# Optimization experiments

Measured on AMD Instinct MI355X. Metric: run time of the kernel, lower is better.

Reference implementation:

```python
import jax, jax.numpy as jnp
import numpy as np

B, L, D, N, NBLK = 16, 2048, 256, 64, 6  # 6 S4D layers: blocks 1,2,3,5 + 2 inner layers of FS4Ddeq


def setup_inputs() -> dict:
    key = jax.random.key(0)
    ks = jax.random.split(key, 12)
    x = jax.random.normal(ks[0], (B, L), dtype=jnp.float32)
    W_emb = jax.random.normal(ks[1], (1, D), dtype=jnp.float32) * 0.1
    b_emb = jnp.zeros((D,), jnp.float32)
    # S4D parameters, stacked over the 6 layers
    log_dt = jax.random.uniform(ks[2], (NBLK, D), minval=float(np.log(1e-3)), maxval=float(np.log(1e-1)), dtype=jnp.float32)
    logAre = jnp.full((NBLK, D, N), float(np.log(0.5)), jnp.float32)
    Aim = jnp.broadcast_to(jnp.pi * jnp.arange(N, dtype=jnp.float32), (NBLK, D, N)) * jnp.ones((NBLK, D, N), jnp.float32)
    Cre = jax.random.normal(ks[3], (NBLK, D, N), dtype=jnp.float32) * (0.5 ** 0.5)
    Cim = jax.random.normal(ks[4], (NBLK, D, N), dtype=jnp.float32) * (0.5 ** 0.5)
    Dskip = jax.random.normal(ks[5], (NBLK, D), dtype=jnp.float32)
    Wout = jax.random.normal(ks[6], (NBLK, D, D), dtype=jnp.float32) / np.sqrt(D)
    bout = jnp.zeros((NBLK, D), jnp.float32)
    gamma = jnp.ones((NBLK, D), jnp.float32)
    beta = jnp.zeros((NBLK, D), jnp.float32)
    # feedforward of the FS4Ddeq block (feed_size=[B,L,emb_dim], feed_act='relu')
    feed_W1 = jax.random.normal(ks[7], (D, D), dtype=jnp.float32) / np.sqrt(D)
    feed_b1 = jnp.zeros((D,), jnp.float32)
    feed_W2 = jax.random.normal(ks[8], (D, D), dtype=jnp.float32) / np.sqrt(D)
    feed_b2 = jnp.zeros((D,), jnp.float32)
    fc_W = jax.random.normal(ks[9], (D, 2), dtype=jnp.float32) / np.sqrt(D)
    fc_b = jnp.zeros((2,), jnp.float32)
    return dict(x=x, W_emb=W_emb, b_emb=b_emb, log_dt=log_dt, logAre=logAre, Aim=Aim,
                Cre=Cre, Cim=Cim, Dskip=Dskip, Wout=Wout, bout=bout, gamma=gamma, beta=beta,
                feed_W1=feed_W1, feed_b1=feed_b1, feed_W2=feed_W2, feed_b2=feed_b2,
                fc_W=fc_W, fc_b=fc_b)


def _s4d_block(h, log_dt, logAre, Aim, Cre, Cim, Dskip, Wout, bout, gamma, beta):
    """Pre-norm (BN eval-mode) -> diagonal SSM (ZOH, FFT conv) -> GELU -> Linear -> residual."""
    _, Lh, _ = h.shape
    z = gamma * h + beta  # BatchNorm in eval mode with identity running stats
    dt = jnp.exp(log_dt)[:, None]                      # [D,1]
    A = -jnp.exp(logAre) + 1j * Aim                    # [D,N] diagonal state matrix
    dtA = dt * A                                       # [D,N]
    C = (Cre + 1j * Cim) * (jnp.exp(dtA) - 1.0) / A    # ZOH-discretized C*B
    # Vandermonde kernel K[d,l] = 2*Re sum_n C[d,n] * exp(dtA[d,n])^l
    vand = jnp.exp(dtA[:, :, None] * jnp.arange(Lh, dtype=jnp.float32))  # [D,N,L]
    K = 2.0 * jnp.einsum('dn,dnl->dl', C, vand).real   # [D,L]
    u = jnp.transpose(z, (0, 2, 1))                    # [B,D,L]
    kf = jnp.fft.rfft(K, n=2 * Lh)
    uf = jnp.fft.rfft(u, n=2 * Lh)
    y = jnp.fft.irfft(uf * kf, n=2 * Lh)[..., :Lh]     # causal conv
    y = y + Dskip[:, None] * u                         # feedthrough D
    y = jax.nn.gelu(jnp.transpose(y, (0, 2, 1)))       # [B,L,D]
    y = jnp.einsum('bld,de->ble', y, Wout) + bout      # output projection
    return y + h                                       # skip connection


def reference(x, W_emb, b_emb, log_dt, logAre, Aim, Cre, Cim, Dskip, Wout, bout,
              gamma, beta, feed_W1, feed_b1, feed_W2, feed_b2, fc_W, fc_b):
    h = x[..., None] @ W_emb + b_emb  # nn.Linear(1, emb_dim): [B,L,D]
    # layers 1,2,3,5: S4D blocks (dropout is identity in eval mode)
    for i in range(4):
        h = _s4d_block(h, log_dt[i], logAre[i], Aim[i], Cre[i], Cim[i],
                       Dskip[i], Wout[i], bout[i], gamma[i], beta[i])
    # layer4: FS4Ddeq_model with layers=2 inner S4D blocks + relu feed net + final relu + skip
    r = h
    for i in (4, 5):
        h = _s4d_block(h, log_dt[i], logAre[i], Aim[i], Cre[i], Cim[i],
                       Dskip[i], Wout[i], bout[i], gamma[i], beta[i])
    h = jax.nn.relu(h @ feed_W1 + feed_b1) @ feed_W2 + feed_b2
    h = jax.nn.relu(h + r)
    mean_y = jnp.mean(h, axis=1)       # [B,D]
    logits = mean_y @ fc_W + fc_b      # [B,2]
    return logits
```

## Files before the change

kernel.cpp:

```cpp
#include <hip/hip_runtime.h>
#include <hip/hip_fp16.h>
#include <math.h>

#define B_ 16
#define L_ 2048
#define D_ 256
#define N_ 64
#define NBLK_ 6
#define LC_ 128
#define NC_ 16

typedef _Float16 half8 __attribute__((ext_vector_type(8)));
typedef float f32x4 __attribute__((ext_vector_type(4)));

__device__ __forceinline__ unsigned short f2h(float f) {
  _Float16 h = (_Float16)f;
  return *(unsigned short*)&h;
}
__device__ __forceinline__ float h2f(unsigned short u) {
  _Float16 h = *(_Float16*)&u;
  return (float)h;
}

__global__ void precompute_kernel(const float* __restrict__ log_dt,
                                  const float* __restrict__ logAre,
                                  const float* __restrict__ Aim,
                                  const float* __restrict__ Cre,
                                  const float* __restrict__ Cim,
                                  float* __restrict__ wbuf,
                                  float* __restrict__ c2buf,
                                  float* __restrict__ wlbuf) {
  int idx = blockIdx.x * blockDim.x + threadIdx.x;
  if (idx >= NBLK_ * D_ * N_) return;
  int blk = idx >> 14;
  int rem = idx & 16383;
  int d = rem >> 6;
  int n = rem & 63;
  float dt   = expf(log_dt[blk * D_ + d]);
  float are  = -expf(logAre[idx]);
  float aim  = Aim[idx];
  float dtar = dt * are, dtai = dt * aim;
  float er = expf(dtar);
  float wr = er * cosf(dtai);
  float wi = er * sinf(dtai);
  float inv = 1.0f / (are * are + aim * aim);
  float wm1r = wr - 1.0f;
  float br = (wm1r * are + wi * aim) * inv;
  float bi = (wi * are - wm1r * aim) * inv;
  float crv = Cre[idx], civ = Cim[idx];
  float c2r = 2.0f * (crv * br - civ * bi);
  float c2i = 2.0f * (crv * bi + civ * br);
  float eL = expf((float)LC_ * dtar);
  float angL = (float)LC_ * dtai;
  float* wb = wbuf + (size_t)((blk << 8) + d) * 128;
  wb[n] = wr; wb[64 + n] = wi;
  float* cb = c2buf + (size_t)((blk << 8) + d) * 128;
  cb[n] = c2r; cb[64 + n] = c2i;
  wlbuf[2 * idx] = eL * cosf(angL); wlbuf[2 * idx + 1] = eL * sinf(angL);
}

__global__ void embed_kernel(const float* __restrict__ x, const float* __restrict__ wemb,
                             const float* __restrict__ bemb, unsigned short* __restrict__ H) {
  int tid = blockIdx.x * blockDim.x + threadIdx.x;
  if (tid >= B_ * L_ * D_) return;
  int d = tid & (D_ - 1);
  int lg = tid >> 8;
  H[tid] = f2h(fmaf(x[lg], wemb[d], bemb[d]));
}

__global__ __launch_bounds__(256) void trans_h_ut(const unsigned short* __restrict__ H,
                                                  unsigned short* __restrict__ UT) {
  __shared__ __align__(16) unsigned short lds[64][136];
  int bi = blockIdx.x;
  int bc = bi >> 2, dq = bi & 3;
  int b = bc >> 4, ch = bc & 15;
  int tid = threadIdx.x;
  const unsigned short* src = H + ((size_t)(b * L_ + ch * 128)) * D_ + dq * 64;
  int tau0 = tid >> 4;
  int dl = (tid & 15) << 2;
  for (int tt = 0; tt < 128; tt += 16) {
    ushort4 v = *(const ushort4*)(src + (size_t)(tt + tau0) * D_ + dl);
    lds[dl + 0][tt + tau0] = v.x;
    lds[dl + 1][tt + tau0] = v.y;
    lds[dl + 2][tt + tau0] = v.z;
    lds[dl + 3][tt + tau0] = v.w;
  }
  __syncthreads();
  int r = tid >> 2, seg = (tid & 3) << 5;
  unsigned short* dst = UT + ((size_t)((dq * 64 + r) * 256 + bc)) * 128 + seg;
  const unsigned short* srow = &lds[r][seg];
  *(uint4*)(dst + 0)  = *(const uint4*)(srow + 0);
  *(uint4*)(dst + 8)  = *(const uint4*)(srow + 8);
  *(uint4*)(dst + 16) = *(const uint4*)(srow + 16);
  *(uint4*)(dst + 24) = *(const uint4*)(srow + 24);
}

__global__ __launch_bounds__(256) void scan_fused(
    const unsigned short* __restrict__ UT,
    const float* __restrict__ WB, const float* __restrict__ C2B,
    const float* __restrict__ WLB,
    const float* __restrict__ gamma_, const float* __restrict__ beta_,
    const float* __restrict__ dskip,
    unsigned short* __restrict__ GT, int blk) {
  __shared__ __align__(16) unsigned short SLl[256 * 136];
  __shared__ __align__(16) unsigned short Bm1[128 * 136];
  __shared__ __align__(16) unsigned short Bm2[128 * 136];
  __shared__ __align__(16) unsigned short AsB[128 * 40];
  __shared__ float wc[256];
  __shared__ float Kt[128];
  __shared__ float Pb[128];
  __shared__ float Sb[128];
  _Float16* As = (_Float16*)AsB;
  int d = blockIdx.x;
  int tid = threadIdx.x, lane = tid & 63, w = tid >> 6;
  int wm = (w & 1) << 6, wn = (w >> 1) << 6;
  int r = tid & 127, sg = (tid >> 7) << 4;
  int cn = lane & 15, rq = lane >> 4;
  int ko = (lane >> 4) << 3;
  const unsigned short* Au = UT + (size_t)d * 256 * 128;

  if (tid < 128) wc[tid] = WB[(size_t)((blk << 8) + d) * 128 + tid];
  else           wc[tid] = C2B[(size_t)((blk << 8) + d) * 128 + (tid - 128)];
  __syncthreads();
  int n = tid & 63, tj = tid >> 6;
  float gd = gamma_[blk * D_ + d], bd = beta_[blk * D_ + d], dsk = dskip[blk * D_ + d];
  {
    float wr = wc[n], wi = wc[64 + n];
    float c2r = wc[128 + n], c2i = wc[192 + n];
    int j0 = tj << 5;
    float pr = 1.f, pi = 0.f, br = wr, bi = wi;
    int e = j0;
    while (e) {
      if (e & 1) { float tt = pr * br - pi * bi; pi = pr * bi + pi * br; pr = tt; }
      float t2 = br * br - bi * bi; bi = 2.f * br * bi; br = t2;
      e >>= 1;
    }
    for (int k2 = 0; k2 < 32; ++k2) {
      int j = j0 + k2;
      Bm1[n * 136 + (127 - j)]        = f2h(gd * pr);
      Bm1[(64 + n) * 136 + (127 - j)] = f2h(-gd * pi);
      float qr = pr * wr - pi * wi, qi = pr * wi + pi * wr;
      Bm2[j * 136 + n]      = f2h(c2r * qr - c2i * qi);
      Bm2[j * 136 + 64 + n] = f2h(c2r * qi + c2i * qr);
      float kc = c2r * pr - c2i * pi;
#pragma unroll
      for (int off = 1; off < 64; off <<= 1) kc += __shfl_xor(kc, off);
      if (n == 0) Kt[j] = kc + (j == 0 ? dsk : 0.f);
      pr = qr; pi = qi;
    }
  }
  if (tid < 64) {
    const float* wlp = WLB + (((size_t)((blk << 8) + d)) * 64 + tid) * 2;
    float wlr = wlp[0], wli = wlp[1];
    float nr = wlr - 1.f, ni = wli;
    float dr2 = wc[tid] - 1.f, di = wc[64 + tid];
    float iv = 1.f / (dr2 * dr2 + di * di);
    Sb[tid]      = bd * ((nr * dr2 + ni * di) * iv);
    Sb[64 + tid] = bd * (-((ni * dr2 - nr * di) * iv));
  }
  __syncthreads();
  if (tid < 128) {
    float ps = 0.f;
    for (int t2 = 0; t2 <= tid; ++t2) ps += Kt[t2];
    Pb[tid] = bd * ps;
  }

  for (int mh = 0; mh < 2; ++mh) {
    const unsigned short* Ab = Au + (size_t)(mh << 7) * 128;
    f32x4 acc[4][4];
#pragma unroll
    for (int a = 0; a < 4; ++a)
#pragma unroll
      for (int b2 = 0; b2 < 4; ++b2) acc[a][b2] = (f32x4){0.f, 0.f, 0.f, 0.f};
    uint4 a0 = *(const uint4*)(Ab + (size_t)r * 128 + sg);
    uint4 a1 = *(const uint4*)(Ab + (size_t)r * 128 + sg + 8);
    for (int kc = 0; kc < 128; kc += 32) {
      __syncthreads();
      *(uint4*)&As[r * 40 + sg] = a0; *(uint4*)&As[r * 40 + sg + 8] = a1;
      __syncthreads();
      if (kc < 96) {
        a0 = *(const uint4*)(Ab + (size_t)r * 128 + kc + 32 + sg);
        a1 = *(const uint4*)(Ab + (size_t)r * 128 + kc + 32 + sg + 8);
      }
      half8 af[4], bf4[4];
#pragma unroll
      for (int mf = 0; mf < 4; ++mf) af[mf] = *(const half8*)&As[(wm + (mf << 4) + cn) * 40 + ko];
#pragma unroll
      for (int nf = 0; nf < 4; ++nf)
        bf4[nf] = *(const half8*)((const _Float16*)Bm1 + (wn + (nf << 4) + cn) * 136 + kc + ko);
#pragma unroll
      for (int mf = 0; mf < 4; ++mf)
#pragma unroll
        for (int nf = 0; nf < 4; ++nf)
          acc[mf][nf] = __builtin_amdgcn_mfma_f32_16x16x32_f16(af[mf], bf4[nf], acc[mf][nf], 0, 0, 0);
    }
#pragma unroll
    for (int nf = 0; nf < 4; ++nf) {
      int nl = wn + (nf << 4) + cn;
      float sb = Sb[nl];
#pragma unroll
      for (int mf = 0; mf < 4; ++mf)
#pragma unroll
        for (int rr = 0; rr < 4; ++rr) {
          int row = (mh << 7) + wm + (mf << 4) + (rq << 2) + rr;
          SLl[row * 136 + nl] = f2h(acc[mf][nf][rr] + sb);
        }
    }
  }
  __syncthreads();

  for (int task = tid; task < 1024; task += 256) {
    int b = task >> 6, nn = task & 63;
    const float* wlp = WLB + (((size_t)((blk << 8) + d)) * 64 + nn) * 2;
    float wlr = wlp[0], wli = wlp[1];
    float Sr = 0.f, Sj = 0.f;
    for (int c = 0; c < NC_; ++c) {
      int row = (b << 4) + c;
      float tr2 = h2f(SLl[row * 136 + nn]);
      float tj2 = h2f(SLl[row * 136 + 64 + nn]);
      SLl[row * 136 + nn]      = f2h(Sr);
      SLl[row * 136 + 64 + nn] = f2h(Sj);
      float nSr = fmaf(wlr, Sr, fmaf(wli, Sj, tr2));
      Sj = fmaf(-wli, Sr, fmaf(wlr, Sj, tj2));
      Sr = nSr;
    }
  }
  __syncthreads();

  {
    int chunk = tid & 15, rg = tid >> 4;
#pragma unroll
    for (int it = 0; it < 8; ++it) {
      int trow = (it << 4) + rg;
      int tau0 = chunk << 3;
      unsigned short v[8];
#pragma unroll
      for (int i = 0; i < 8; ++i) {
        int tau = tau0 + i;
        v[i] = (tau <= trow) ? f2h(gd * Kt[trow - tau]) : (unsigned short)0;
      }
      *(uint4*)(Bm1 + (size_t)trow * 136 + tau0) = *(uint4*)v;
    }
  }
  __syncthreads();

  for (int mh = 0; mh < 2; ++mh) {
    const unsigned short* Ab = Au + (size_t)(mh << 7) * 128;
    const _Float16* SA = (const _Float16*)SLl + (size_t)(mh << 7) * 136;
    f32x4 acc[4][4];
#pragma unroll
    for (int a = 0; a < 4; ++a)
#pragma unroll
      for (int b2 = 0; b2 < 4; ++b2) acc[a][b2] = (f32x4){0.f, 0.f, 0.f, 0.f};
    uint4 a0 = *(const uint4*)(Ab + (size_t)r * 128 + sg);
    uint4 a1 = *(const uint4*)(Ab + (size_t)r * 128 + sg + 8);
    for (int kb = 0; kb < 8; ++kb) {
      int kc = (kb & 3) << 5;
      half8 af[4], bf4[4];
      if (kb < 4) {
        __syncthreads();
        *(uint4*)&As[r * 40 + sg] = a0; *(uint4*)&As[r * 40 + sg + 8] = a1;
        __syncthreads();
        if (kb < 3) {
          int kc2 = (kb + 1) << 5;
          a0 = *(const uint4*)(Ab + (size_t)r * 128 + kc2 + sg);
          a1 = *(const uint4*)(Ab + (size_t)r * 128 + kc2 + sg + 8);
        }
#pragma unroll
        for (int mf = 0; mf < 4; ++mf) af[mf] = *(const half8*)&As[(wm + (mf << 4) + cn) * 40 + ko];
#pragma unroll
        for (int nf = 0; nf < 4; ++nf)
          bf4[nf] = *(const half8*)((const _Float16*)Bm1 + (wn + (nf << 4) + cn) * 136 + kc + ko);
      } else {
#pragma unroll
        for (int mf = 0; mf < 4; ++mf)
          af[mf] = *(const half8*)&SA[(wm + (mf << 4) + cn) * 136 + kc + ko];
#pragma unroll
        for (int nf = 0; nf < 4; ++nf)
          bf4[nf] = *(const half8*)((const _Float16*)Bm2 + (wn + (nf << 4) + cn) * 136 + kc + ko);
      }
#pragma unroll
      for (int mf = 0; mf < 4; ++mf)
#pragma unroll
        for (int nf = 0; nf < 4; ++nf)
          acc[mf][nf] = __builtin_amdgcn_mfma_f32_16x16x32_f16(af[mf], bf4[nf], acc[mf][nf], 0, 0, 0);
    }
    __syncthreads();
    unsigned short* epi = SLl + (size_t)(mh << 7) * 136;
#pragma unroll
    for (int nf = 0; nf < 4; ++nf) {
      int nl = wn + (nf << 4) + cn;
      float pb2 = Pb[nl];
#pragma unroll
      for (int mf = 0; mf < 4; ++mf)
#pragma unroll
        for (int rr = 0; rr < 4; ++rr) {
          int ml = wm + (mf << 4) + (rq << 2) + rr;
          float xx = acc[mf][nf][rr] + pb2;
          float x3 = xx * xx * xx;
          float inner = 0.7978845608028654f * fmaf(0.044715f, x3, xx);
          float e = __expf(-2.f * fabsf(inner));
          float th = (1.f - e) / (1.f + e);
          th = copysignf(th, inner);
          epi[ml * 136 + nl] = f2h(0.5f * xx * (1.f + th));
        }
    }
    __syncthreads();
    int mr = tid >> 1, hf = (tid & 1) << 6;
    size_t gb = ((size_t)d * 256 + (mh << 7) + mr) * 128 + hf;
#pragma unroll
    for (int k = 0; k < 8; ++k)
      *(uint4*)(GT + gb + k * 8) = *(const uint4*)&epi[mr * 136 + hf + k * 8];
  }
}

__global__ void wprep_kernel(const float* __restrict__ Wout, const float* __restrict__ fW1,
                             const float* __restrict__ fW2, unsigned short* __restrict__ WT) {
  __shared__ float tile[64][65];
  int wv = blockIdx.x >> 4;
  int tk = (blockIdx.x >> 2) & 3;
  int tn = blockIdx.x & 3;
  const float* src = (wv < 6) ? (Wout + (size_t)wv * 65536) : (wv == 6 ? fW1 : fW2);
  int r = threadIdx.x >> 4;
  int c = (threadIdx.x & 15) << 2;
  for (int rr = 0; rr < 64; rr += 16) {
    float4 v = *(const float4*)(src + (size_t)(tk * 64 + r + rr) * 256 + tn * 64 + c);
    tile[r + rr][c] = v.x; tile[r + rr][c + 1] = v.y;
    tile[r + rr][c + 2] = v.z; tile[r + rr][c + 3] = v.w;
  }
  __syncthreads();
  for (int rr = 0; rr < 64; rr += 16) {
    int n = r + rr;
    ushort4 o;
    o.x = f2h(tile[c + 0][n]); o.y = f2h(tile[c + 1][n]);
    o.z = f2h(tile[c + 2][n]); o.w = f2h(tile[c + 3][n]);
    *(ushort4*)(WT + (size_t)wv * 65536 + (size_t)(tn * 64 + n) * 256 + tk * 64 + c) = o;
  }
}

__global__ __launch_bounds__(256, 2) void gemm_gt(const unsigned short* __restrict__ GT,
    const unsigned short* __restrict__ Wt, const float* __restrict__ bias,
    const unsigned short* __restrict__ res, unsigned short* __restrict__ hout,
    unsigned short* __restrict__ ut_next) {
  __shared__ __align__(16) unsigned short smem[18432];
  unsigned short* As = smem;
  unsigned short* Bs = smem + 9216;
  int tid = threadIdx.x;
  int bid = blockIdx.x;
  int bc = bid & 255;
  int m0 = bc * 128, n0 = (bid >> 8) << 7;
  int lane = tid & 63, w = tid >> 6;
  int wm = (w & 1) << 6, wn = (w >> 1) << 6;
  int rb = tid >> 3, cb = (tid & 7) << 3;
  int dr = tid >> 2, sg = (tid & 3) << 5;
  f32x4 acc[4][4];
#pragma unroll
  for (int mf = 0; mf < 4; ++mf)
#pragma unroll
    for (int nf = 0; nf < 4; ++nf) acc[mf][nf] = (f32x4){0.f, 0.f, 0.f, 0.f};

  uint4 gv[4], bv[4];
  {
    const uint4* grow = (const uint4*)(GT + ((size_t)(dr * 256 + bc)) * 128 + sg);
    gv[0] = grow[0]; gv[1] = grow[1]; gv[2] = grow[2]; gv[3] = grow[3];
#pragma unroll
    for (int rr = 0; rr < 4; ++rr)
      bv[rr] = *(const uint4*)(Wt + (size_t)(n0 + rb + rr * 32) * 256 + cb);
  }
  for (int kb = 0; kb < 4; ++kb) {
    __syncthreads();
    const unsigned short* pv = (const unsigned short*)gv;
#pragma unroll
    for (int i = 0; i < 32; ++i) As[(sg + i) * 72 + dr] = pv[i];
#pragma unroll
    for (int rr = 0; rr < 4; ++rr) *(uint4*)&Bs[(rb + rr * 32) * 72 + cb] = bv[rr];
    __syncthreads();
    if (kb < 3) {
      int k0 = (kb + 1) << 6;
      const uint4* grow = (const uint4*)(GT + ((size_t)((k0 + dr) * 256 + bc)) * 128 + sg);
      gv[0] = grow[0]; gv[1] = grow[1]; gv[2] = grow[2]; gv[3] = grow[3];
#pragma unroll
      for (int rr = 0; rr < 4; ++rr)
        bv[rr] = *(const uint4*)(Wt + (size_t)(n0 + rb + rr * 32) * 256 + k0 + cb);
    }
#pragma unroll
    for (int kw = 0; kw < 2; ++kw) {
      int ko = (kw << 5) + ((lane >> 4) << 3);
      half8 af[4], bfr[4];
#pragma unroll
      for (int mf = 0; mf < 4; ++mf)
        af[mf] = *(const half8*)&As[(wm + (mf << 4) + (lane & 15)) * 72 + ko];
#pragma unroll
      for (int nf = 0; nf < 4; ++nf)
        bfr[nf] = *(const half8*)&Bs[(wn + (nf << 4) + (lane & 15)) * 72 + ko];
#pragma unroll
      for (int mf = 0; mf < 4; ++mf)
#pragma unroll
        for (int nf = 0; nf < 4; ++nf)
          acc[mf][nf] = __builtin_amdgcn_mfma_f32_16x16x32_f16(af[mf], bfr[nf], acc[mf][nf], 0, 0, 0);
    }
  }
  int cn = lane & 15, rq = lane >> 4;
  __syncthreads();
  unsigned short* epi = smem;
#pragma unroll
  for (int nf = 0; nf < 4; ++nf) {
    int nl = wn + (nf << 4) + cn;
    float bv2 = bias[n0 + nl];
#pragma unroll
    for (int mf = 0; mf < 4; ++mf)
#pragma unroll
      for (int r = 0; r < 4; ++r) {
        int ml = wm + (mf << 4) + (rq << 2) + r;
        float v = acc[mf][nf][r] + bv2 + h2f(res[(size_t)(m0 + ml) * 256 + n0 + nl]);
        epi[ml * 136 + nl] = f2h(v);
      }
  }
  __syncthreads();
  {
    int mr = tid >> 1, hf = (tid & 1) << 6;
    unsigned short* dst = hout + (size_t)(m0 + mr) * 256 + n0 + hf;
    const unsigned short* srow = epi + mr * 136 + hf;
#pragma unroll
    for (int k = 0; k < 8; ++k) *(uint4*)(dst + k * 8) = *(const uint4*)(srow + k * 8);
  }
  if (ut_next) {
    int nl = tid >> 1, h2 = (tid & 1) << 6;
    unsigned short* dst = ut_next + ((size_t)(n0 + nl) * 256 + bc) * 128 + h2;
#pragma unroll
    for (int k = 0; k < 8; ++k) {
      unsigned short v8[8];
#pragma unroll
      for (int e = 0; e < 8; ++e) v8[e] = epi[(h2 + k * 8 + e) * 136 + nl];
      *(uint4*)(dst + k * 8) = *(uint4*)v8;
    }
  }
}

__global__ __launch_bounds__(256, 2) void gemm_ffn(const unsigned short* __restrict__ A,
    const unsigned short* __restrict__ Wt, const float* __restrict__ bias,
    const unsigned short* __restrict__ res, unsigned short* __restrict__ outp) {
  __shared__ __align__(16) unsigned short smem[18432];
  unsigned short* As = smem;
  unsigned short* Bs = smem + 9216;
  int tid = threadIdx.x;
  int bid = blockIdx.x;
  int m0 = (bid & 255) << 7, n0 = (bid >> 8) << 7;
  int lane = tid & 63, w = tid >> 6;
  int wm = (w & 1) << 6, wn = (w >> 1) << 6;
  int r0 = tid >> 3;
  int c0 = (tid & 7) << 3;
  f32x4 acc[4][4];
#pragma unroll
  for (int mf = 0; mf < 4; ++mf)
#pragma unroll
    for (int nf = 0; nf < 4; ++nf) acc[mf][nf] = (f32x4){0.f, 0.f, 0.f, 0.f};

  uint4 av[4], bv[4];
#pragma unroll
  for (int rr = 0; rr < 4; ++rr) {
    int r = r0 + rr * 32;
    av[rr] = *(const uint4*)(A + (size_t)(m0 + r) * 256 + c0);
    bv[rr] = *(const uint4*)(Wt + (size_t)(n0 + r) * 256 + c0);
  }
  for (int kb = 0; kb < 4; ++kb) {
    __syncthreads();
#pragma unroll
    for (int rr = 0; rr < 4; ++rr) {
      int r = r0 + rr * 32;
      *(uint4*)&As[r * 72 + c0] = av[rr];
      *(uint4*)&Bs[r * 72 + c0] = bv[rr];
    }
    __syncthreads();
    if (kb < 3) {
      int k0 = (kb + 1) << 6;
#pragma unroll
      for (int rr = 0; rr < 4; ++rr) {
        int r = r0 + rr * 32;
        av[rr] = *(const uint4*)(A + (size_t)(m0 + r) * 256 + k0 + c0);
        bv[rr] = *(const uint4*)(Wt + (size_t)(n0 + r) * 256 + k0 + c0);
      }
    }
#pragma unroll
    for (int kw = 0; kw < 2; ++kw) {
      int ko = (kw << 5) + ((lane >> 4) << 3);
      half8 af[4], bfr[4];
#pragma unroll
      for (int mf = 0; mf < 4; ++mf)
        af[mf] = *(const half8*)&As[(wm + (mf << 4) + (lane & 15)) * 72 + ko];
#pragma unroll
      for (int nf = 0; nf < 4; ++nf)
        bfr[nf] = *(const half8*)&Bs[(wn + (nf << 4) + (lane & 15)) * 72 + ko];
#pragma unroll
      for (int mf = 0; mf < 4; ++mf)
#pragma unroll
        for (int nf = 0; nf < 4; ++nf)
          acc[mf][nf] = __builtin_amdgcn_mfma_f32_16x16x32_f16(af[mf], bfr[nf], acc[mf][nf], 0, 0, 0);
    }
  }
  int cn = lane & 15, rq = lane >> 4;
  __syncthreads();
  unsigned short* epi = smem;
#pragma unroll
  for (int nf = 0; nf < 4; ++nf) {
    int nl = wn + (nf << 4) + cn;
#pragma unroll
    for (int r = 0; r < 4; ++r) {
#pragma unroll
      for (int mf = 0; mf < 4; ++mf) {
        int ml = wm + (mf << 4) + (rq << 2) + r;
        epi[ml * 136 + nl] = f2h(acc[mf][nf][r]);
      }
    }
  }
  __syncthreads();
  int mr = tid >> 1, hf = (tid & 1) << 6;
  unsigned short* dst = outp + (size_t)(m0 + mr) * 256 + n0 + hf;
#pragma unroll
  for (int k = 0; k < 8; ++k) {
    uint4 c = *(const uint4*)&epi[mr * 136 + hf + k * 8];
    uint4 rv = (uint4){0, 0, 0, 0};
    if (res) rv = *(const uint4*)(res + (size_t)(m0 + mr) * 256 + n0 + hf + k * 8);
    const unsigned short* cp = (const unsigned short*)&c;
    const unsigned short* rp = (const unsigned short*)&rv;
    unsigned short o8[8];
#pragma unroll
    for (int e = 0; e < 8; ++e) {
      float v = h2f(cp[e]) + bias[n0 + hf + k * 8 + e];
      if (res) v += h2f(rp[e]);
      o8[e] = f2h(fmaxf(v, 0.f));
    }
    *(uint4*)(dst + k * 8) = *(uint4*)o8;
  }
}

__global__ void head1_kernel(const unsigned short* __restrict__ H, float* __restrict__ part) {
  int b = blockIdx.x, ls = blockIdx.y, d = threadIdx.x;
  const unsigned short* p = H + ((size_t)(b * L_ + ls * 128)) * D_ + d;
  float sum = 0.f;
  for (int l = 0; l < 128; ++l) sum += h2f(p[(size_t)l * D_]);
  part[(b * 16 + ls) * D_ + d] = sum;
}

__global__ void head2_kernel(const float* __restrict__ part, const float* __restrict__ fcW,
                             const float* __restrict__ fcb, float* __restrict__ out) {
  int b = blockIdx.x, d = threadIdx.x;
  float sum = 0.f;
  for (int i = 0; i < 16; ++i) sum += part[(b * 16 + i) * D_ + d];
  __shared__ float meanv[D_];
  meanv[d] = sum * (1.0f / (float)L_);
  __syncthreads();
  if (d < 2) {
    float accv = fcb[d];
    for (int k = 0; k < D_; ++k) accv = fmaf(meanv[k], fcW[k * 2 + d], accv);
    out[b * 2 + d] = accv;
  }
}

extern "C" void kernel_launch(void* const* d_in, const int* in_sizes, int n_in,
                              void* d_out, int out_size, void* d_ws, size_t ws_size,
                              hipStream_t stream) {
  const float* x      = (const float*)d_in[0];
  const float* W_emb  = (const float*)d_in[1];
  const float* b_emb  = (const float*)d_in[2];
  const float* log_dt = (const float*)d_in[3];
  const float* logAre = (const float*)d_in[4];
  const float* Aim    = (const float*)d_in[5];
  const float* Cre    = (const float*)d_in[6];
  const float* Cim    = (const float*)d_in[7];
  const float* Dskip  = (const float*)d_in[8];
  const float* Wout   = (const float*)d_in[9];
  const float* bout   = (const float*)d_in[10];
  const float* gamma_ = (const float*)d_in[11];
  const float* beta_  = (const float*)d_in[12];
  const float* fW1    = (const float*)d_in[13];
  const float* fb1    = (const float*)d_in[14];
  const float* fW2    = (const float*)d_in[15];
  const float* fb2    = (const float*)d_in[16];
  const float* fcW    = (const float*)d_in[17];
  const float* fcb    = (const float*)d_in[18];
  float* outp = (float*)d_out;

  const size_t HSZ = (size_t)B_ * L_ * D_;
  float* WB     = (float*)d_ws;
  float* C2B    = WB + (size_t)NBLK_ * D_ * 128;
  float* WLB    = C2B + (size_t)NBLK_ * D_ * 128;
  unsigned short* H   = (unsigned short*)(WLB + (size_t)NBLK_ * D_ * N_ * 2);
  unsigned short* R   = H + HSZ;
  unsigned short* UT  = R + HSZ;
  unsigned short* GT  = UT + HSZ;
  unsigned short* Gbf = GT;
  unsigned short* WT  = GT + HSZ;

  precompute_kernel<<<(NBLK_ * D_ * N_ + 255) / 256, 256, 0, stream>>>(
      log_dt, logAre, Aim, Cre, Cim, WB, C2B, WLB);
  wprep_kernel<<<128, 256, 0, stream>>>(Wout, fW1, fW2, WT);
  embed_kernel<<<(B_ * L_ * D_ + 255) / 256, 256, 0, stream>>>(x, W_emb, b_emb, H);
  trans_h_ut<<<1024, 256, 0, stream>>>(H, UT);

  const unsigned short* hin_t[6]  = {H, H, H, H, R, H};
  unsigned short*       hout_t[6] = {H, H, H, R, H, H};
  for (int i = 0; i < 6; ++i) {
    scan_fused<<<256, 256, 0, stream>>>(UT, WB, C2B, WLB, gamma_, beta_, Dskip, GT, i);
    gemm_gt<<<512, 256, 0, stream>>>(
        GT, WT + (size_t)i * 65536, bout + i * D_, hin_t[i], hout_t[i],
        (i < 5) ? UT : nullptr);
  }
  gemm_ffn<<<512, 256, 0, stream>>>(H, WT + (size_t)6 * 65536, fb1, nullptr, Gbf);
  gemm_ffn<<<512, 256, 0, stream>>>(Gbf, WT + (size_t)7 * 65536, fb2, R, H);
  head1_kernel<<<dim3(16, 16), 256, 0, stream>>>(H, WB);
  head2_kernel<<<16, 256, 0, stream>>>(WB, fcW, fcb, outp);
}
```

Before: 610.5 us.

## Widen scan_fused to 512 threads covering both row halves at once

```diff
diff --git a/kernel.cpp b/kernel.cpp
--- a/kernel.cpp
+++ b/kernel.cpp
@@ -95,7 +95,7 @@
   *(uint4*)(dst + 24) = *(const uint4*)(srow + 24);
 }
 
-__global__ __launch_bounds__(256) void scan_fused(
+__global__ __launch_bounds__(512) void scan_fused(
     const unsigned short* __restrict__ UT,
     const float* __restrict__ WB, const float* __restrict__ C2B,
     const float* __restrict__ WLB,
@@ -105,7 +105,7 @@
   __shared__ __align__(16) unsigned short SLl[256 * 136];
   __shared__ __align__(16) unsigned short Bm1[128 * 136];
   __shared__ __align__(16) unsigned short Bm2[128 * 136];
-  __shared__ __align__(16) unsigned short AsB[128 * 40];
+  __shared__ __align__(16) unsigned short AsB[256 * 40];
   __shared__ float wc[256];
   __shared__ float Kt[128];
   __shared__ float Pb[128];
@@ -113,21 +113,22 @@
   _Float16* As = (_Float16*)AsB;
   int d = blockIdx.x;
   int tid = threadIdx.x, lane = tid & 63, w = tid >> 6;
-  int wm = (w & 1) << 6, wn = (w >> 1) << 6;
-  int r = tid & 127, sg = (tid >> 7) << 4;
+  int wm = (w & 3) << 6;
+  int wn = (w >> 2) << 6;
+  int r = tid & 255, sg = (tid >> 8) << 4;
   int cn = lane & 15, rq = lane >> 4;
-  int ko = (lane >> 4) << 3;
+  int ko = rq << 3;
   const unsigned short* Au = UT + (size_t)d * 256 * 128;
 
   if (tid < 128) wc[tid] = WB[(size_t)((blk << 8) + d) * 128 + tid];
-  else           wc[tid] = C2B[(size_t)((blk << 8) + d) * 128 + (tid - 128)];
-  __syncthreads();
-  int n = tid & 63, tj = tid >> 6;
+  else if (tid < 256) wc[tid] = C2B[(size_t)((blk << 8) + d) * 128 + (tid - 128)];
+  __syncthreads();
+  int n = tid & 63;
   float gd = gamma_[blk * D_ + d], bd = beta_[blk * D_ + d], dsk = dskip[blk * D_ + d];
   {
     float wr = wc[n], wi = wc[64 + n];
     float c2r = wc[128 + n], c2i = wc[192 + n];
-    int j0 = tj << 5;
+    int j0 = (tid >> 6) << 4;
     float pr = 1.f, pi = 0.f, br = wr, bi = wi;
     int e = j0;
     while (e) {
@@ -135,7 +136,7 @@
       float t2 = br * br - bi * bi; bi = 2.f * br * bi; br = t2;
       e >>= 1;
     }
-    for (int k2 = 0; k2 < 32; ++k2) {
+    for (int k2 = 0; k2 < 16; ++k2) {
       int j = j0 + k2;
       Bm1[n * 136 + (127 - j)]        = f2h(gd * pr);
       Bm1[(64 + n) * 136 + (127 - j)] = f2h(-gd * pi);
@@ -165,22 +166,21 @@
     Pb[tid] = bd * ps;
   }
 
-  for (int mh = 0; mh < 2; ++mh) {
-    const unsigned short* Ab = Au + (size_t)(mh << 7) * 128;
+  {
     f32x4 acc[4][4];
 #pragma unroll
     for (int a = 0; a < 4; ++a)
 #pragma unroll
       for (int b2 = 0; b2 < 4; ++b2) acc[a][b2] = (f32x4){0.f, 0.f, 0.f, 0.f};
-    uint4 a0 = *(const uint4*)(Ab + (size_t)r * 128 + sg);
-    uint4 a1 = *(const uint4*)(Ab + (size_t)r * 128 + sg + 8);
+    uint4 a0 = *(const uint4*)(Au + (size_t)r * 128 + sg);
+    uint4 a1 = *(const uint4*)(Au + (size_t)r * 128 + sg + 8);
     for (int kc = 0; kc < 128; kc += 32) {
       __syncthreads();
       *(uint4*)&As[r * 40 + sg] = a0; *(uint4*)&As[r * 40 + sg + 8] = a1;
       __syncthreads();
       if (kc < 96) {
-        a0 = *(const uint4*)(Ab + (size_t)r * 128 + kc + 32 + sg);
-        a1 = *(const uint4*)(Ab + (size_t)r * 128 + kc + 32 + sg + 8);
+        a0 = *(const uint4*)(Au + (size_t)r * 128 + kc + 32 + sg);
+        a1 = *(const uint4*)(Au + (size_t)r * 128 + kc + 32 + sg + 8);
       }
       half8 af[4], bf4[4];
 #pragma unroll
@@ -202,14 +202,14 @@
       for (int mf = 0; mf < 4; ++mf)
 #pragma unroll
         for (int rr = 0; rr < 4; ++rr) {
-          int row = (mh << 7) + wm + (mf << 4) + (rq << 2) + rr;
+          int row = wm + (mf << 4) + (rq << 2) + rr;
           SLl[row * 136 + nl] = f2h(acc[mf][nf][rr] + sb);
         }
     }
   }
   __syncthreads();
 
-  for (int task = tid; task < 1024; task += 256) {
+  for (int task = tid; task < 1024; task += 512) {
     int b = task >> 6, nn = task & 63;
     const float* wlp = WLB + (((size_t)((blk << 8) + d)) * 64 + nn) * 2;
     float wlr = wlp[0], wli = wlp[1];
@@ -230,8 +230,8 @@
   {
     int chunk = tid & 15, rg = tid >> 4;
 #pragma unroll
-    for (int it = 0; it < 8; ++it) {
-      int trow = (it << 4) + rg;
+    for (int it = 0; it < 4; ++it) {
+      int trow = (it << 5) + rg;
       int tau0 = chunk << 3;
       unsigned short v[8];
 #pragma unroll
@@ -244,16 +244,14 @@
   }
   __syncthreads();
 
-  for (int mh = 0; mh < 2; ++mh) {
-    const unsigned short* Ab = Au + (size_t)(mh << 7) * 128;
-    const _Float16* SA = (const _Float16*)SLl + (size_t)(mh << 7) * 136;
+  {
     f32x4 acc[4][4];
 #pragma unroll
     for (int a = 0; a < 4; ++a)
 #pragma unroll
       for (int b2 = 0; b2 < 4; ++b2) acc[a][b2] = (f32x4){0.f, 0.f, 0.f, 0.f};
-    uint4 a0 = *(const uint4*)(Ab + (size_t)r * 128 + sg);
-    uint4 a1 = *(const uint4*)(Ab + (size_t)r * 128 + sg + 8);
+    uint4 a0 = *(const uint4*)(Au + (size_t)r * 128 + sg);
+    uint4 a1 = *(const uint4*)(Au + (size_t)r * 128 + sg + 8);
     for (int kb = 0; kb < 8; ++kb) {
       int kc = (kb & 3) << 5;
       half8 af[4], bf4[4];
@@ -263,8 +261,8 @@
         __syncthreads();
         if (kb < 3) {
           int kc2 = (kb + 1) << 5;
-          a0 = *(const uint4*)(Ab + (size_t)r * 128 + kc2 + sg);
-          a1 = *(const uint4*)(Ab + (size_t)r * 128 + kc2 + sg + 8);
+          a0 = *(const uint4*)(Au + (size_t)r * 128 + kc2 + sg);
+          a1 = *(const uint4*)(Au + (size_t)r * 128 + kc2 + sg + 8);
         }
 #pragma unroll
         for (int mf = 0; mf < 4; ++mf) af[mf] = *(const half8*)&As[(wm + (mf << 4) + cn) * 40 + ko];
@@ -274,7 +272,7 @@
       } else {
 #pragma unroll
         for (int mf = 0; mf < 4; ++mf)
-          af[mf] = *(const half8*)&SA[(wm + (mf << 4) + cn) * 136 + kc + ko];
+          af[mf] = *(const half8*)((const _Float16*)SLl + (wm + (mf << 4) + cn) * 136 + kc + ko);
 #pragma unroll
         for (int nf = 0; nf < 4; ++nf)
           bf4[nf] = *(const half8*)((const _Float16*)Bm2 + (wn + (nf << 4) + cn) * 136 + kc + ko);
@@ -286,7 +284,7 @@
           acc[mf][nf] = __builtin_amdgcn_mfma_f32_16x16x32_f16(af[mf], bf4[nf], acc[mf][nf], 0, 0, 0);
     }
     __syncthreads();
-    unsigned short* epi = SLl + (size_t)(mh << 7) * 136;
+    unsigned short* epi = SLl;
 #pragma unroll
     for (int nf = 0; nf < 4; ++nf) {
       int nl = wn + (nf << 4) + cn;
@@ -307,7 +305,7 @@
     }
     __syncthreads();
     int mr = tid >> 1, hf = (tid & 1) << 6;
-    size_t gb = ((size_t)d * 256 + (mh << 7) + mr) * 128 + hf;
+    size_t gb = ((size_t)d * 256 + mr) * 128 + hf;
 #pragma unroll
     for (int k = 0; k < 8; ++k)
       *(uint4*)(GT + gb + k * 8) = *(const uint4*)&epi[mr * 136 + hf + k * 8];
@@ -601,7 +599,7 @@
   const unsigned short* hin_t[6]  = {H, H, H, H, R, H};
   unsigned short*       hout_t[6] = {H, H, H, R, H, H};
   for (int i = 0; i < 6; ++i) {
-    scan_fused<<<256, 256, 0, stream>>>(UT, WB, C2B, WLB, gamma_, beta_, Dskip, GT, i);
+    scan_fused<<<256, 512, 0, stream>>>(UT, WB, C2B, WLB, gamma_, beta_, Dskip, GT, i);
     gemm_gt<<<512, 256, 0, stream>>>(
         GT, WT + (size_t)i * 65536, bout + i * D_, hin_t[i], hout_t[i],
         (i < 5) ? UT : nullptr);
```

New measurement: 566.8 us. -7.2%, faster.
